# Optimization experiments

Measured on AMD Instinct MI355X. Metric: run time of the kernel, lower is better.

The kernel has to match this reference:

```python
import jax, jax.numpy as jnp
import numpy as np

EPS = 1e-5

def _ln(x, g, b):
    m = jnp.mean(x, axis=-1, keepdims=True)
    v = jnp.var(x, axis=-1, keepdims=True)
    return (x - m) * jax.lax.rsqrt(v + EPS) * g + b

def _gelu(x):
    return jax.nn.gelu(x, approximate=False)  # torch nn.GELU default is exact erf

def setup_inputs() -> dict:
    key = jax.random.key(0)
    B, N, D, H = 4, 1024, 128, 12
    HID = H * D
    ks = jax.random.split(key, 16)
    s = lambda k, sh, fan: jax.random.normal(k, sh, jnp.float32) * (fan ** -0.5)
    return {
        "x": jax.random.normal(ks[0], (B, N, D), jnp.float32),
        # project: LN(D) -> Linear(D,HID) -> GELU -> Linear(HID,HID)
        "ln1_g": jnp.ones((D,), jnp.float32), "ln1_b": jnp.zeros((D,), jnp.float32),
        "W1": s(ks[1], (D, HID), D), "b1": jnp.zeros((HID,), jnp.float32),
        "W2": s(ks[2], (HID, HID), HID), "b2": jnp.zeros((HID,), jnp.float32),
        # shared Attention(inc=D, outc=D)
        "aln_g": jnp.ones((D,), jnp.float32), "aln_b": jnp.zeros((D,), jnp.float32),
        "Wqkv": s(ks[3], (D, 3 * D), D), "bqkv": jnp.zeros((3 * D,), jnp.float32),
        "Wl": s(ks[4], (D, D), D), "bl": jnp.zeros((D,), jnp.float32),
        # out_proj: LN(HID) -> Linear(HID, D) -> GELU
        "lno_g": jnp.ones((HID,), jnp.float32), "lno_b": jnp.zeros((HID,), jnp.float32),
        "Wo": s(ks[5], (HID, D), HID), "bo": jnp.zeros((D,), jnp.float32),
    }

def reference(x, ln1_g, ln1_b, W1, b1, W2, b2,
              aln_g, aln_b, Wqkv, bqkv, Wl, bl,
              lno_g, lno_b, Wo, bo):
    B, N, D = x.shape
    # project (dropout is identity in eval mode)
    h = _ln(x, ln1_g, ln1_b)
    h = _gelu(h @ W1 + b1)
    h = h @ W2 + b2                      # [B, N, H*D]
    H = h.shape[-1] // D
    # chunk along last dim into H features of width D; fold heads into batch
    f = h.reshape(B, N, H, D).transpose(0, 2, 1, 3).reshape(B * H, N, D)
    # shared Attention applied to each head-chunk
    a = _ln(f, aln_g, aln_b)
    qkv = a @ Wqkv + bqkv
    q, k, v = jnp.split(qkv, 3, axis=-1)
    scores = jax.nn.softmax(jnp.einsum('bnd,bmd->bnm', q, k) * (D ** -0.5), axis=-1)
    o = jnp.einsum('bnm,bmd->bnd', scores, v)
    o = o @ Wl + bl
    o = _gelu(o + f)                     # [B*H, N, D]
    # concat heads back along last dim
    feats = o.reshape(B, H, N, D).transpose(0, 2, 1, 3).reshape(B, N, H * D)
    out = _gelu(_ln(feats, lno_g, lno_b) @ Wo + bo)
    return out
```

## Files before the change

### kernel.cpp

```cpp
#include <hip/hip_runtime.h>
#include <stdint.h>

typedef unsigned short u16;
typedef __attribute__((ext_vector_type(8))) short short8;
typedef __attribute__((ext_vector_type(4))) float floatx4;

__device__ inline float b2f(u16 u) {
  union { uint32_t i; float f; } x; x.i = ((uint32_t)u) << 16; return x.f;
}
__device__ inline u16 f2b(float f) {
  union { float f; uint32_t i; } x; x.f = f;
  uint32_t r = (x.i + 0x7FFFu + ((x.i >> 16) & 1u)) >> 16;
  return (u16)r;
}
__device__ inline float gelu_f(float v) {
  return 0.5f * v * (1.0f + erff(v * 0.70710678118654752440f));
}

#define MFMA16(a, b, c) __builtin_amdgcn_mfma_f32_16x16x32_bf16((a), (b), (c), 0, 0, 0)

__device__ __forceinline__ void gl2lds16(const u16* g, u16* l) {
  __builtin_amdgcn_global_load_lds(
      (const __attribute__((address_space(1))) uint32_t*)(uintptr_t)g,
      (__attribute__((address_space(3))) uint32_t*)(uint32_t)(uintptr_t)l,
      16, 0, 0);
}

__global__ __launch_bounds__(256)
void tpose_all_kernel(const float* __restrict__ W1, const float* __restrict__ W2,
                      const float* __restrict__ Wqkv, const float* __restrict__ Wl,
                      const float* __restrict__ Wo,
                      u16* __restrict__ w1t, u16* __restrict__ w2t,
                      u16* __restrict__ wqkvt, u16* __restrict__ wlt,
                      u16* __restrict__ wot) {
  int id = blockIdx.x;
  const float* src; u16* dst; int R, C, bx, by;
  if (id < 2304)      { src = W2;   dst = w2t;   R = 1536; C = 1536; bx = (id % 48) * 32; by = (id / 48) * 32; }
  else if (id < 2496) { id -= 2304; src = W1;   dst = w1t;   R = 128;  C = 1536; bx = (id % 48) * 32; by = (id / 48) * 32; }
  else if (id < 2688) { id -= 2496; src = Wo;   dst = wot;   R = 1536; C = 128;  bx = (id % 4) * 32;  by = (id / 4) * 32; }
  else if (id < 2736) { id -= 2688; src = Wqkv; dst = wqkvt; R = 128;  C = 384;  bx = (id % 12) * 32; by = (id / 12) * 32; }
  else                { id -= 2736; src = Wl;   dst = wlt;   R = 128;  C = 128;  bx = (id % 4) * 32;  by = (id / 4) * 32; }
  __shared__ u16 t[32][33];
  int tx = threadIdx.x & 31, ty = threadIdx.x >> 5;
  for (int i = 0; i < 32; i += 8)
    t[ty + i][tx] = f2b(src[(size_t)(by + ty + i) * C + bx + tx]);
  __syncthreads();
  for (int i = 0; i < 32; i += 8)
    dst[(size_t)(bx + ty + i) * R + by + tx] = t[tx][ty + i];
}

__global__ __launch_bounds__(256)
void vtrans_kernel(const u16* __restrict__ qkv, u16* __restrict__ vT) {
  int bh = blockIdx.y;
  int n0 = blockIdx.x * 32;
  int b = bh / 12, h = bh % 12;
  const int rs = 12 * 384;
  const u16* vp = qkv + (((size_t)b * 1024) * 12 + h) * 384 + 256;
  __shared__ u16 t[4][32][33];
  int tx = threadIdx.x & 31, ty = threadIdx.x >> 5;
  for (int dt = 0; dt < 4; dt++)
    for (int i = 0; i < 32; i += 8)
      t[dt][ty + i][tx] = vp[(size_t)(n0 + ty + i) * rs + dt * 32 + tx];
  __syncthreads();
  u16* dp = vT + (size_t)bh * 128 * 1024 + n0;
  for (int dt = 0; dt < 4; dt++)
    for (int i = 0; i < 32; i += 8)
      dp[(size_t)(dt * 32 + ty + i) * 1024 + tx] = t[dt][tx][ty + i];
}

__global__ __launch_bounds__(256)
void ln128_f32_kernel(const float* __restrict__ X, const float* __restrict__ g,
                      const float* __restrict__ bb, u16* __restrict__ Y) {
  int tid = threadIdx.x, w = tid >> 6, lane = tid & 63;
  int row = blockIdx.x * 4 + w;
  const float* xr = X + (size_t)row * 128;
  float2 xv = *(const float2*)(xr + lane * 2);
  float x0 = xv.x, x1 = xv.y;
  float s = x0 + x1, s2 = x0 * x0 + x1 * x1;
  for (int m = 1; m < 64; m <<= 1) { s += __shfl_xor(s, m, 64); s2 += __shfl_xor(s2, m, 64); }
  float mean = s * (1.0f / 128.0f);
  float var = s2 * (1.0f / 128.0f) - mean * mean;
  float rstd = 1.0f / sqrtf(var + 1e-5f);
  float2 gv = *(const float2*)(g + lane * 2);
  float2 bv = *(const float2*)(bb + lane * 2);
  float y0 = (x0 - mean) * rstd * gv.x + bv.x;
  float y1 = (x1 - mean) * rstd * gv.y + bv.y;
  *(uint32_t*)(Y + (size_t)row * 128 + lane * 2) =
      (uint32_t)f2b(y0) | ((uint32_t)f2b(y1) << 16);
}

__global__ __launch_bounds__(256)
void ln128_bf16_kernel(const u16* __restrict__ X, const float* __restrict__ g,
                       const float* __restrict__ bb, u16* __restrict__ Y) {
  int tid = threadIdx.x, w = tid >> 6, lane = tid & 63;
  int row = blockIdx.x * 4 + w;
  const u16* xr = X + (size_t)row * 128;
  uint32_t u = *(const uint32_t*)(xr + lane * 2);
  float x0 = b2f(u & 0xffff), x1 = b2f(u >> 16);
  float s = x0 + x1, s2 = x0 * x0 + x1 * x1;
  for (int m = 1; m < 64; m <<= 1) { s += __shfl_xor(s, m, 64); s2 += __shfl_xor(s2, m, 64); }
  float mean = s * (1.0f / 128.0f);
  float var = s2 * (1.0f / 128.0f) - mean * mean;
  float rstd = 1.0f / sqrtf(var + 1e-5f);
  float2 gv = *(const float2*)(g + lane * 2);
  float2 bv = *(const float2*)(bb + lane * 2);
  float y0 = (x0 - mean) * rstd * gv.x + bv.x;
  float y1 = (x1 - mean) * rstd * gv.y + bv.y;
  *(uint32_t*)(Y + (size_t)row * 128 + lane * 2) =
      (uint32_t)f2b(y0) | ((uint32_t)f2b(y1) << 16);
}

__global__ __launch_bounds__(256)
void ln1536_kernel(const u16* __restrict__ X, const float* __restrict__ g,
                   const float* __restrict__ bb, u16* __restrict__ Y) {
  int row = blockIdx.x, tid = threadIdx.x;
  const u16* xr = X + (size_t)row * 1536;
  uint32_t u0 = *(const uint32_t*)(xr + tid * 6);
  uint32_t u1 = *(const uint32_t*)(xr + tid * 6 + 2);
  uint32_t u2 = *(const uint32_t*)(xr + tid * 6 + 4);
  float v[6] = { b2f(u0 & 0xffff), b2f(u0 >> 16), b2f(u1 & 0xffff),
                 b2f(u1 >> 16),    b2f(u2 & 0xffff), b2f(u2 >> 16) };
  float s = 0.f, s2 = 0.f;
  for (int j = 0; j < 6; j++) { s += v[j]; s2 += v[j] * v[j]; }
  for (int m = 1; m < 64; m <<= 1) { s += __shfl_xor(s, m, 64); s2 += __shfl_xor(s2, m, 64); }
  __shared__ float red[8];
  int w = tid >> 6, lane = tid & 63;
  if (lane == 0) { red[w] = s; red[4 + w] = s2; }
  __syncthreads();
  s = red[0] + red[1] + red[2] + red[3];
  s2 = red[4] + red[5] + red[6] + red[7];
  float mean = s * (1.0f / 1536.0f);
  float var = s2 * (1.0f / 1536.0f) - mean * mean;
  float rstd = 1.0f / sqrtf(var + 1e-5f);
  uint32_t o[3];
  for (int p = 0; p < 3; p++) {
    int c = tid * 6 + p * 2;
    float y0 = (v[p * 2] - mean) * rstd * g[c] + bb[c];
    float y1 = (v[p * 2 + 1] - mean) * rstd * g[c + 1] + bb[c + 1];
    o[p] = (uint32_t)f2b(y0) | ((uint32_t)f2b(y1) << 16);
  }
  u16* yr = Y + (size_t)row * 1536 + tid * 6;
  *(uint32_t*)(yr) = o[0];
  *(uint32_t*)(yr + 2) = o[1];
  *(uint32_t*)(yr + 4) = o[2];
}

template <int GELU, int RES, typename OUTT>
__global__ __launch_bounds__(256)
void gemm_kernel(const u16* __restrict__ A, const u16* __restrict__ BT,
                 const float* __restrict__ bias, const u16* __restrict__ res,
                 OUTT* __restrict__ C, int M, int N, int K) {
  __shared__ __align__(16) u16 abuf[128 * 32];
  __shared__ __align__(16) u16 bbuf[128 * 32];
  int tid = threadIdx.x;
  int w = tid >> 6, lane = tid & 63, ln = lane & 15, quad = lane >> 4;
  int bm = blockIdx.x * 128, bn = blockIdx.y * 128;
  int wr = w >> 1, wc = w & 1;
  floatx4 acc[4][4] = {};
  for (int k0 = 0; k0 < K; k0 += 32) {
    __syncthreads();
    for (int rd = 0; rd < 2; rd++) {
      int c = tid + rd * 256;
      int row = c >> 2, col = (c & 3) * 8;
      gl2lds16(A + (size_t)(bm + row) * K + k0 + col, abuf + c * 8);
      gl2lds16(BT + (size_t)(bn + row) * K + k0 + col, bbuf + c * 8);
    }
    __syncthreads();
    short8 af[4], bf[4];
    for (int i = 0; i < 4; i++)
      af[i] = *(const short8*)(abuf + (wr * 64 + i * 16 + ln) * 32 + quad * 8);
    for (int j = 0; j < 4; j++)
      bf[j] = *(const short8*)(bbuf + (wc * 64 + j * 16 + ln) * 32 + quad * 8);
    for (int i = 0; i < 4; i++)
      for (int j = 0; j < 4; j++)
        acc[i][j] = MFMA16(af[i], bf[j], acc[i][j]);
  }
  for (int i = 0; i < 4; i++) {
    int row0 = bm + wr * 64 + i * 16 + quad * 4;
    for (int j = 0; j < 4; j++) {
      int col = bn + wc * 64 + j * 16 + ln;
      float bv = bias[col];
      for (int r = 0; r < 4; r++) {
        float v = acc[i][j][r] + bv;
        if (RES) v += b2f(res[(size_t)(row0 + r) * N + col]);
        if (GELU) v = gelu_f(v);
        if constexpr (sizeof(OUTT) == 2)
          C[(size_t)(row0 + r) * N + col] = f2b(v);
        else
          C[(size_t)(row0 + r) * N + col] = v;
      }
    }
  }
}

template <int GELU, int RES, typename OUTT>
__global__ __launch_bounds__(256)
void gemm64_kernel(const u16* __restrict__ A, const u16* __restrict__ BT,
                   const float* __restrict__ bias, const u16* __restrict__ res,
                   OUTT* __restrict__ C, int M, int N, int K) {
  __shared__ __align__(16) u16 abuf[64 * 32];
  __shared__ __align__(16) u16 bbuf[128 * 32];
  int tid = threadIdx.x;
  int w = tid >> 6, lane = tid & 63, ln = lane & 15, quad = lane >> 4;
  int bm = blockIdx.x * 64, bn = blockIdx.y * 128;
  floatx4 acc[4][2] = {};
  for (int k0 = 0; k0 < K; k0 += 32) {
    __syncthreads();
    for (int rd = 0; rd < 2; rd++) {
      int c = tid + rd * 256;
      int row = c >> 2, col = (c & 3) * 8;
      gl2lds16(BT + (size_t)(bn + row) * K + k0 + col, bbuf + c * 8);
    }
    {
      int c = tid;
      int row = c >> 2, col = (c & 3) * 8;
      gl2lds16(A + (size_t)(bm + row) * K + k0 + col, abuf + c * 8);
    }
    __syncthreads();
    short8 af[4], bf[2];
    for (int i = 0; i < 4; i++)
      af[i] = *(const short8*)(abuf + (i * 16 + ln) * 32 + quad * 8);
    for (int j = 0; j < 2; j++)
      bf[j] = *(const short8*)(bbuf + (w * 32 + j * 16 + ln) * 32 + quad * 8);
    for (int i = 0; i < 4; i++)
      for (int j = 0; j < 2; j++)
        acc[i][j] = MFMA16(af[i], bf[j], acc[i][j]);
  }
  for (int i = 0; i < 4; i++) {
    int row0 = bm + i * 16 + quad * 4;
    for (int j = 0; j < 2; j++) {
      int col = bn + w * 32 + j * 16 + ln;
      float bv = bias[col];
      for (int r = 0; r < 4; r++) {
        float v = acc[i][j][r] + bv;
        if (RES) v += b2f(res[(size_t)(row0 + r) * N + col]);
        if (GELU) v = gelu_f(v);
        if constexpr (sizeof(OUTT) == 2)
          C[(size_t)(row0 + r) * N + col] = f2b(v);
        else
          C[(size_t)(row0 + r) * N + col] = v;
      }
    }
  }
}

__global__ __launch_bounds__(256)
void gemm64_part_kernel(const u16* __restrict__ A, const u16* __restrict__ BT,
                        float* __restrict__ pws, int Kfull, int kspan) {
  __shared__ __align__(16) u16 abuf[64 * 32];
  __shared__ __align__(16) u16 bbuf[128 * 32];
  int tid = threadIdx.x;
  int w = tid >> 6, lane = tid & 63, ln = lane & 15, quad = lane >> 4;
  int bm = blockIdx.x * 64;
  int kbeg = blockIdx.y * kspan, kend = kbeg + kspan;
  float* Cp = pws + (size_t)blockIdx.y * 4096 * 128;
  floatx4 acc[4][2] = {};
  for (int k0 = kbeg; k0 < kend; k0 += 32) {
    __syncthreads();
    for (int rd = 0; rd < 2; rd++) {
      int c = tid + rd * 256;
      int row = c >> 2, col = (c & 3) * 8;
      gl2lds16(BT + (size_t)row * Kfull + k0 + col, bbuf + c * 8);
    }
    {
      int c = tid;
      int row = c >> 2, col = (c & 3) * 8;
      gl2lds16(A + (size_t)(bm + row) * Kfull + k0 + col, abuf + c * 8);
    }
    __syncthreads();
    short8 af[4], bf[2];
    for (int i = 0; i < 4; i++)
      af[i] = *(const short8*)(abuf + (i * 16 + ln) * 32 + quad * 8);
    for (int j = 0; j < 2; j++)
      bf[j] = *(const short8*)(bbuf + (w * 32 + j * 16 + ln) * 32 + quad * 8);
    for (int i = 0; i < 4; i++)
      for (int j = 0; j < 2; j++)
        acc[i][j] = MFMA16(af[i], bf[j], acc[i][j]);
  }
  for (int i = 0; i < 4; i++) {
    int row0 = bm + i * 16 + quad * 4;
    for (int j = 0; j < 2; j++) {
      int col = w * 32 + j * 16 + ln;
      for (int r = 0; r < 4; r++)
        Cp[(size_t)(row0 + r) * 128 + col] = acc[i][j][r];
    }
  }
}

__global__ __launch_bounds__(256)
void combine_wo_kernel(const float* __restrict__ p, const float* __restrict__ bias,
                       float* __restrict__ out) {
  int i = blockIdx.x * 256 + threadIdx.x;
  const int SZ = 4096 * 128;
  float v = p[i] + p[i + SZ] + p[i + 2 * SZ] + p[i + 3 * SZ] + bias[i & 127];
  out[i] = gelu_f(v);
}

__global__ __launch_bounds__(256)
void attn_kernel(const u16* __restrict__ qkv, const u16* __restrict__ vT,
                 u16* __restrict__ obuf) {
  int blk = blockIdx.x;
  int qt = blk & 15, bh = blk >> 4;
  int b = bh / 12, hh = bh % 12;
  int tid = threadIdx.x, w = tid >> 6, lane = tid & 63, ln = lane & 15, quad = lane >> 4;
  __shared__ __align__(16) u16 kbuf[4 * 32 * 32];
  __shared__ __align__(16) u16 vbuf[128 * 32];
  __shared__ __align__(16) u16 pbuf[4][16 * 40];
  const int rs = 12 * 384;
  size_t base = (((size_t)b * 1024) * 12 + hh) * 384;
  const u16* qp = qkv + base;
  const u16* kp = qkv + base + 128;
  const u16* vp = vT + (size_t)bh * 128 * 1024;

  short8 onesb;
  {
    short v = (ln == 0) ? (short)0x3F80 : (short)0;
    for (int j = 0; j < 8; j++) onesb[j] = v;
  }

  int qrow = qt * 64 + w * 16 + ln;
  short8 qf[4];
  for (int st = 0; st < 4; st++)
    qf[st] = *(const short8*)(qp + (size_t)qrow * rs + st * 32 + quad * 8);

  floatx4 o[9] = {};
  const float K2 = 0.08838834764831845f * 1.4426950408889634f;

  for (int kt = 0; kt < 32; kt++) {
    __syncthreads();
    for (int it = 0; it < 2; it++) {
      int c = it * 256 + tid;
      int st = c >> 7, key = (c >> 2) & 31, cc = c & 3;
      gl2lds16(kp + (size_t)(kt * 32 + key) * rs + st * 32 + cc * 8, kbuf + c * 8);
      int d = c >> 2;
      gl2lds16(vp + (size_t)d * 1024 + kt * 32 + cc * 8, vbuf + c * 8);
    }
    __syncthreads();

    floatx4 s[2] = {};
    for (int t = 0; t < 2; t++)
      for (int st = 0; st < 4; st++) {
        short8 bk = *(const short8*)(kbuf + st * 1024 + (t * 16 + ln) * 32 + quad * 8);
        s[t] = MFMA16(qf[st], bk, s[t]);
      }
    for (int r = 0; r < 4; r++) {
      float p0 = exp2f(s[0][r] * K2), p1 = exp2f(s[1][r] * K2);
      int prow = (quad * 4 + r) * 40;
      pbuf[w][prow + ln] = f2b(p0);
      pbuf[w][prow + 16 + ln] = f2b(p1);
    }
    short8 ap = *(const short8*)(&pbuf[w][ln * 40 + quad * 8]);
    for (int dt = 0; dt < 8; dt++) {
      short8 bv = *(const short8*)(vbuf + (dt * 16 + ln) * 32 + quad * 8);
      o[dt] = MFMA16(ap, bv, o[dt]);
    }
    o[8] = MFMA16(ap, onesb, o[8]);
  }

  for (int r = 0; r < 4; r++) {
    float l = __shfl(o[8][r], lane & 48);
    float inv = 1.0f / l;
    int n = qt * 64 + w * 16 + quad * 4 + r;
    size_t ob = ((((size_t)b * 1024 + n) * 12) + hh) * 128;
    for (int dt = 0; dt < 8; dt++)
      obuf[ob + dt * 16 + ln] = f2b(o[dt][r] * inv);
  }
}

extern "C" void kernel_launch(void* const* d_in, const int* in_sizes, int n_in,
                              void* d_out, int out_size, void* d_ws, size_t ws_size,
                              hipStream_t stream) {
  (void)in_sizes; (void)n_in; (void)out_size; (void)ws_size;
  const float* x    = (const float*)d_in[0];
  const float* ln1g = (const float*)d_in[1];
  const float* ln1b = (const float*)d_in[2];
  const float* W1   = (const float*)d_in[3];
  const float* b1   = (const float*)d_in[4];
  const float* W2   = (const float*)d_in[5];
  const float* b2   = (const float*)d_in[6];
  const float* alng = (const float*)d_in[7];
  const float* alnb = (const float*)d_in[8];
  const float* Wqkv = (const float*)d_in[9];
  const float* bqkv = (const float*)d_in[10];
  const float* Wl   = (const float*)d_in[11];
  const float* bl   = (const float*)d_in[12];
  const float* lnog = (const float*)d_in[13];
  const float* lnob = (const float*)d_in[14];
  const float* Wo   = (const float*)d_in[15];
  const float* bo   = (const float*)d_in[16];
  float* out = (float*)d_out;

  char* ws = (char*)d_ws;
  size_t off = 0;
  auto alloc = [&](size_t elems) { u16* p = (u16*)(ws + off); off += elems * sizeof(u16); return p; };
  u16* w1t   = alloc((size_t)1536 * 128);
  u16* w2t   = alloc((size_t)1536 * 1536);
  u16* wqkvt = alloc((size_t)384 * 128);
  u16* wlt   = alloc((size_t)128 * 128);
  u16* wot   = alloc((size_t)128 * 1536);
  u16* lnx   = alloc((size_t)4096 * 128);
  u16* h1    = alloc((size_t)4096 * 1536);
  u16* h2    = alloc((size_t)4096 * 1536);
  u16* aln   = alloc((size_t)49152 * 128);
  u16* qkv   = alloc((size_t)49152 * 384);
  u16* obuf = h1;
  u16* vT = aln;
  u16* feats = aln;
  u16* lnf = qkv;
  float* pws = (float*)h1;

  dim3 T(256);
  tpose_all_kernel<<<dim3(2752), T, 0, stream>>>(W1, W2, Wqkv, Wl, Wo,
                                                 w1t, w2t, wqkvt, wlt, wot);
  ln128_f32_kernel<<<dim3(4096 / 4), T, 0, stream>>>(x, ln1g, ln1b, lnx);
  gemm64_kernel<1, 0, u16><<<dim3(4096 / 64, 1536 / 128), T, 0, stream>>>(
      lnx, w1t, b1, nullptr, h1, 4096, 1536, 128);
  gemm64_kernel<0, 0, u16><<<dim3(4096 / 64, 1536 / 128), T, 0, stream>>>(
      h1, w2t, b2, nullptr, h2, 4096, 1536, 1536);
  ln128_bf16_kernel<<<dim3(49152 / 4), T, 0, stream>>>(h2, alng, alnb, aln);
  gemm_kernel<0, 0, u16><<<dim3(49152 / 128, 384 / 128), T, 0, stream>>>(
      aln, wqkvt, bqkv, nullptr, qkv, 49152, 384, 128);
  vtrans_kernel<<<dim3(1024 / 32, 48), T, 0, stream>>>(qkv, vT);
  attn_kernel<<<dim3(768), T, 0, stream>>>(qkv, vT, obuf);
  gemm64_kernel<1, 1, u16><<<dim3(49152 / 64, 1), T, 0, stream>>>(
      obuf, wlt, bl, h2, feats, 49152, 128, 128);
  ln1536_kernel<<<dim3(4096), T, 0, stream>>>(feats, lnog, lnob, lnf);
  gemm64_part_kernel<<<dim3(4096 / 64, 4), T, 0, stream>>>(lnf, wot, pws, 1536, 384);
  combine_wo_kernel<<<dim3(4096 * 128 / 256), T, 0, stream>>>(pws, bo, out);
}
```

Baseline: 272.8 us.

## Double K-step per sync in W2 GEMM and attention, remap attention blocks per XCD

```diff
diff --git a/kernel.cpp b/kernel.cpp
--- a/kernel.cpp
+++ b/kernel.cpp
@@ -244,6 +244,65 @@
   }
 }
 
+template <int GELU, int RES, typename OUTT>
+__global__ __launch_bounds__(256)
+void gemm64b_kernel(const u16* __restrict__ A, const u16* __restrict__ BT,
+                    const float* __restrict__ bias, const u16* __restrict__ res,
+                    OUTT* __restrict__ C, int M, int N, int K) {
+  __shared__ __align__(16) u16 abuf[2 * 64 * 32];
+  __shared__ __align__(16) u16 bbuf[2 * 128 * 32];
+  int tid = threadIdx.x;
+  int w = tid >> 6, lane = tid & 63, ln = lane & 15, quad = lane >> 4;
+  int bm = blockIdx.x * 64, bn = blockIdx.y * 128;
+  floatx4 acc[4][2] = {};
+  for (int k0 = 0; k0 < K; k0 += 64) {
+    __syncthreads();
+    for (int ks = 0; ks < 2; ks++) {
+      {
+        int c = tid;
+        int row = c >> 2, cc = c & 3;
+        gl2lds16(A + (size_t)(bm + row) * K + k0 + ks * 32 + cc * 8,
+                 abuf + ks * 2048 + c * 8);
+      }
+      for (int rd = 0; rd < 2; rd++) {
+        int c = tid + rd * 256;
+        int row = c >> 2, cc = c & 3;
+        gl2lds16(BT + (size_t)(bn + row) * K + k0 + ks * 32 + cc * 8,
+                 bbuf + ks * 4096 + c * 8);
+      }
+    }
+    __syncthreads();
+    short8 af[2][4], bf[2][2];
+    for (int ks = 0; ks < 2; ks++) {
+      for (int i = 0; i < 4; i++)
+        af[ks][i] = *(const short8*)(abuf + ks * 2048 + (i * 16 + ln) * 32 + quad * 8);
+      for (int j = 0; j < 2; j++)
+        bf[ks][j] = *(const short8*)(bbuf + ks * 4096 + (w * 32 + j * 16 + ln) * 32 + quad * 8);
+    }
+    for (int i = 0; i < 4; i++)
+      for (int j = 0; j < 2; j++) {
+        acc[i][j] = MFMA16(af[0][i], bf[0][j], acc[i][j]);
+        acc[i][j] = MFMA16(af[1][i], bf[1][j], acc[i][j]);
+      }
+  }
+  for (int i = 0; i < 4; i++) {
+    int row0 = bm + i * 16 + quad * 4;
+    for (int j = 0; j < 2; j++) {
+      int col = bn + w * 32 + j * 16 + ln;
+      float bv = bias[col];
+      for (int r = 0; r < 4; r++) {
+        float v = acc[i][j][r] + bv;
+        if (RES) v += b2f(res[(size_t)(row0 + r) * N + col]);
+        if (GELU) v = gelu_f(v);
+        if constexpr (sizeof(OUTT) == 2)
+          C[(size_t)(row0 + r) * N + col] = f2b(v);
+        else
+          C[(size_t)(row0 + r) * N + col] = v;
+      }
+    }
+  }
+}
+
 __global__ __launch_bounds__(256)
 void gemm64_part_kernel(const u16* __restrict__ A, const u16* __restrict__ BT,
                         float* __restrict__ pws, int Kfull, int kspan) {
@@ -300,12 +359,14 @@
 void attn_kernel(const u16* __restrict__ qkv, const u16* __restrict__ vT,
                  u16* __restrict__ obuf) {
   int blk = blockIdx.x;
-  int qt = blk & 15, bh = blk >> 4;
+  int xcd = blk & 7, slot = blk >> 3;
+  int bh = xcd * 6 + (slot >> 4);
+  int qt = slot & 15;
   int b = bh / 12, hh = bh % 12;
   int tid = threadIdx.x, w = tid >> 6, lane = tid & 63, ln = lane & 15, quad = lane >> 4;
-  __shared__ __align__(16) u16 kbuf[4 * 32 * 32];
-  __shared__ __align__(16) u16 vbuf[128 * 32];
-  __shared__ __align__(16) u16 pbuf[4][16 * 40];
+  __shared__ __align__(16) u16 kbuf[4 * 64 * 32];
+  __shared__ __align__(16) u16 vbuf[2 * 128 * 32];
+  __shared__ __align__(16) u16 pbuf[4][16 * 72];
   const int rs = 12 * 384;
   size_t base = (((size_t)b * 1024) * 12 + hh) * 384;
   const u16* qp = qkv + base;
@@ -326,35 +387,38 @@
   floatx4 o[9] = {};
   const float K2 = 0.08838834764831845f * 1.4426950408889634f;
 
-  for (int kt = 0; kt < 32; kt++) {
-    __syncthreads();
-    for (int it = 0; it < 2; it++) {
+  for (int kt = 0; kt < 16; kt++) {
+    __syncthreads();
+    for (int it = 0; it < 4; it++) {
       int c = it * 256 + tid;
-      int st = c >> 7, key = (c >> 2) & 31, cc = c & 3;
-      gl2lds16(kp + (size_t)(kt * 32 + key) * rs + st * 32 + cc * 8, kbuf + c * 8);
-      int d = c >> 2;
-      gl2lds16(vp + (size_t)d * 1024 + kt * 32 + cc * 8, vbuf + c * 8);
-    }
-    __syncthreads();
-
-    floatx4 s[2] = {};
-    for (int t = 0; t < 2; t++)
+      int st = c >> 8, key = (c >> 2) & 63, cc = c & 3;
+      gl2lds16(kp + (size_t)(kt * 64 + key) * rs + st * 32 + cc * 8, kbuf + c * 8);
+      int kf = c >> 9, d = (c >> 2) & 127;
+      gl2lds16(vp + (size_t)d * 1024 + kt * 64 + kf * 32 + cc * 8, vbuf + c * 8);
+    }
+    __syncthreads();
+
+    floatx4 s[4] = {};
+    for (int t = 0; t < 4; t++)
       for (int st = 0; st < 4; st++) {
-        short8 bk = *(const short8*)(kbuf + st * 1024 + (t * 16 + ln) * 32 + quad * 8);
+        short8 bk = *(const short8*)(kbuf + st * 2048 + (t * 16 + ln) * 32 + quad * 8);
         s[t] = MFMA16(qf[st], bk, s[t]);
       }
     for (int r = 0; r < 4; r++) {
-      float p0 = exp2f(s[0][r] * K2), p1 = exp2f(s[1][r] * K2);
-      int prow = (quad * 4 + r) * 40;
-      pbuf[w][prow + ln] = f2b(p0);
-      pbuf[w][prow + 16 + ln] = f2b(p1);
-    }
-    short8 ap = *(const short8*)(&pbuf[w][ln * 40 + quad * 8]);
-    for (int dt = 0; dt < 8; dt++) {
-      short8 bv = *(const short8*)(vbuf + (dt * 16 + ln) * 32 + quad * 8);
-      o[dt] = MFMA16(ap, bv, o[dt]);
-    }
-    o[8] = MFMA16(ap, onesb, o[8]);
+      int prow = (quad * 4 + r) * 72;
+      pbuf[w][prow + ln]      = f2b(exp2f(s[0][r] * K2));
+      pbuf[w][prow + 16 + ln] = f2b(exp2f(s[1][r] * K2));
+      pbuf[w][prow + 32 + ln] = f2b(exp2f(s[2][r] * K2));
+      pbuf[w][prow + 48 + ln] = f2b(exp2f(s[3][r] * K2));
+    }
+    for (int kf = 0; kf < 2; kf++) {
+      short8 ap = *(const short8*)(&pbuf[w][ln * 72 + kf * 32 + quad * 8]);
+      for (int dt = 0; dt < 8; dt++) {
+        short8 bv = *(const short8*)(vbuf + kf * 4096 + (dt * 16 + ln) * 32 + quad * 8);
+        o[dt] = MFMA16(ap, bv, o[dt]);
+      }
+      o[8] = MFMA16(ap, onesb, o[8]);
+    }
   }
 
   for (int r = 0; r < 4; r++) {
@@ -415,7 +479,7 @@
   ln128_f32_kernel<<<dim3(4096 / 4), T, 0, stream>>>(x, ln1g, ln1b, lnx);
   gemm64_kernel<1, 0, u16><<<dim3(4096 / 64, 1536 / 128), T, 0, stream>>>(
       lnx, w1t, b1, nullptr, h1, 4096, 1536, 128);
-  gemm64_kernel<0, 0, u16><<<dim3(4096 / 64, 1536 / 128), T, 0, stream>>>(
+  gemm64b_kernel<0, 0, u16><<<dim3(4096 / 64, 1536 / 128), T, 0, stream>>>(
       h1, w2t, b2, nullptr, h2, 4096, 1536, 1536);
   ln128_bf16_kernel<<<dim3(49152 / 4), T, 0, stream>>>(h2, alng, alnb, aln);
   gemm_kernel<0, 0, u16><<<dim3(49152 / 128, 384 / 128), T, 0, stream>>>(
```

Measured after the change: 261.7 us. 1.04x faster.
